# Performance work log

Hardware: AMD Instinct MI355X
Metric: run time of the kernel (lower is better)

## Reference

```python
import jax, jax.numpy as jnp
import numpy as np

EMBED_DIM = 1024
NUM_HEADS = 16
HEAD_DIM = EMBED_DIM // NUM_HEADS


def setup_inputs() -> dict:
    key = jax.random.key(0)
    k1, k2, k3, k4, k5 = jax.random.split(key, 5)
    B, T, C = 2, 2048, EMBED_DIM
    s = 1.0 / np.sqrt(C)
    return {
        "x": jax.random.normal(k1, (B, T, C), dtype=jnp.float32),
        "W_qkv": jax.random.normal(k2, (C, 3 * C), dtype=jnp.float32) * s,
        "b_qkv": jnp.zeros((3 * C,), dtype=jnp.float32),
        "W_out": jax.random.normal(k3, (C, C), dtype=jnp.float32) * s,
        "b_out": jnp.zeros((C,), dtype=jnp.float32),
    }


def reference(x, W_qkv, b_qkv, W_out, b_out):
    B, T, C = x.shape
    H, D = NUM_HEADS, HEAD_DIM
    qkv = x @ W_qkv + b_qkv                       # [B, T, 3C]
    q, k, v = jnp.split(qkv, 3, axis=-1)
    # [B, H, T, D]
    q = q.reshape(B, T, H, D).transpose(0, 2, 1, 3)
    k = k.reshape(B, T, H, D).transpose(0, 2, 1, 3)
    v = v.reshape(B, T, H, D).transpose(0, 2, 1, 3)
    scores = jnp.einsum("bhqd,bhkd->bhqk", q, k) / np.sqrt(D)  # [B,H,T,T]
    causal = jnp.tril(jnp.ones((T, T), dtype=bool))
    scores = jnp.where(causal[None, None], scores, -jnp.inf)
    weights = jax.nn.softmax(scores, axis=-1)
    out = jnp.einsum("bhqk,bhkd->bhqd", weights, v)  # [B,H,T,D]
    out = out.transpose(0, 2, 1, 3).reshape(B, T, C)
    return out @ W_out + b_out
```

## Files before the change

### kernel.cpp

```cpp
#include <hip/hip_runtime.h>
#include <stdint.h>

typedef unsigned short u16t;
typedef __attribute__((ext_vector_type(8))) short bf16x8;
typedef __attribute__((ext_vector_type(4))) float f32x4;

#define DEV __device__ __forceinline__

DEV u16t f2bf(float f) {
  union { float f; unsigned u; } v; v.f = f;
  unsigned r = v.u + 0x7FFFu + ((v.u >> 16) & 1u);
  return (u16t)(r >> 16);
}

DEV unsigned cvtpk(float a, float b) {
  unsigned r;
  asm("v_cvt_pk_bf16_f32 %0, %1, %2" : "=v"(r) : "v"(a), "v"(b));
  return r;
}

DEV void glds16(const void* g, void* l) {
  __builtin_amdgcn_global_load_lds((const __attribute__((address_space(1))) void*)g,
                                   (__attribute__((address_space(3))) void*)l, 16, 0, 0);
}

__global__ __launch_bounds__(256) void k_cast_x(const float* __restrict__ x,
                                                u16t* __restrict__ xb, int n) {
  int i = (blockIdx.x * 256 + threadIdx.x) * 8;
  if (i >= n) return;
  const float4* p = (const float4*)(x + i);
  float4 a = p[0], b = p[1];
  union { u16t h[8]; int4 v; } o;
  o.h[0] = f2bf(a.x); o.h[1] = f2bf(a.y); o.h[2] = f2bf(a.z); o.h[3] = f2bf(a.w);
  o.h[4] = f2bf(b.x); o.h[5] = f2bf(b.y); o.h[6] = f2bf(b.z); o.h[7] = f2bf(b.w);
  *(int4*)(xb + i) = o.v;
}

__global__ __launch_bounds__(256) void k_transpose_cast(const float* __restrict__ src,
                                                        u16t* __restrict__ dst,
                                                        int R, int C) {
  __shared__ u16t tile[64][65];
  int c0 = blockIdx.x * 64, r0 = blockIdx.y * 64;
  int tid = threadIdx.x;
#pragma unroll
  for (int i = 0; i < 16; i++) {
    int idx = tid + i * 256;
    int r = idx >> 6, c = idx & 63;
    tile[c][r] = f2bf(src[(size_t)(r0 + r) * C + (c0 + c)]);
  }
  __syncthreads();
#pragma unroll
  for (int i = 0; i < 16; i++) {
    int idx = tid + i * 256;
    int rr = idx >> 6, cc = idx & 63;
    dst[(size_t)(c0 + rr) * R + (r0 + cc)] = tile[rr][cc];
  }
}

template <int K>
DEV void gemm_mainloop(const u16t* __restrict__ A, const u16t* __restrict__ Bt,
                       int m0, int n0, u16t* ldsA, u16t* ldsB, f32x4 acc[4][4]) {
  const int tid = threadIdx.x;
  const int lane = tid & 63;
  const int wid = tid >> 6;
  const int wm = wid >> 1, wn = wid & 1;
#pragma unroll
  for (int i = 0; i < 4; i++)
#pragma unroll
    for (int j = 0; j < 4; j++) acc[i][j] = f32x4{0.f, 0.f, 0.f, 0.f};

  char* lA = (char*)ldsA;
  char* lB = (char*)ldsB;

  for (int k0 = 0; k0 < K; k0 += 32) {
#pragma unroll
    for (int j = 0; j < 2; j++) {
      int g = wid * 64 + lane + j * 256;
      int row = g >> 2;
      int cb = (g & 3) * 16;
      glds16((const char*)(A + (size_t)(m0 + row) * K + k0) + cb,
             lA + j * 4096 + wid * 1024);
      glds16((const char*)(Bt + (size_t)(n0 + row) * K + k0) + cb,
             lB + j * 4096 + wid * 1024);
    }
    __syncthreads();
    bf16x8 af[4], bfr[4];
    const int lr = lane & 15;
    const int ko = (lane >> 4) * 8;
#pragma unroll
    for (int f = 0; f < 4; f++) {
      af[f]  = *(const bf16x8*)(ldsA + (wm * 64 + f * 16 + lr) * 32 + ko);
      bfr[f] = *(const bf16x8*)(ldsB + (wn * 64 + f * 16 + lr) * 32 + ko);
    }
#pragma unroll
    for (int i = 0; i < 4; i++)
#pragma unroll
      for (int j = 0; j < 4; j++)
        acc[i][j] = __builtin_amdgcn_mfma_f32_16x16x32_bf16(af[i], bfr[j], acc[i][j], 0, 0, 0);
    __syncthreads();
  }
}

__global__ __launch_bounds__(256) void k_gemm_qkv(const u16t* __restrict__ xb,
                                                  const u16t* __restrict__ wt,
                                                  const float* __restrict__ bias,
                                                  u16t* __restrict__ q,
                                                  u16t* __restrict__ kk,
                                                  u16t* __restrict__ vt) {
  __shared__ u16t ldsA[128 * 32];
  __shared__ u16t ldsB[128 * 32];
  __shared__ u16t ldsE[4][64 * 64];
  const int m0 = blockIdx.x * 128, n0 = blockIdx.y * 128;
  f32x4 acc[4][4];
  gemm_mainloop<1024>(xb, wt, m0, n0, ldsA, ldsB, acc);

  const int lane = threadIdx.x & 63, wid = threadIdx.x >> 6;
  const int wm = wid >> 1, wn = wid & 1;
  const int nbase = n0 + wn * 64;
  const int which = nbase >> 10;
  const int hb = (nbase & 1023) >> 6;
  const int bb = m0 >> 11;
  const int t0 = (m0 & 2047) + wm * 64;
  const int bh = bb * 16 + hb;
  u16t* eb = ldsE[wid];
#pragma unroll
  for (int fm = 0; fm < 4; fm++) {
#pragma unroll
    for (int fn = 0; fn < 4; fn++) {
      float bv = bias[nbase + fn * 16 + (lane & 15)];
#pragma unroll
      for (int i = 0; i < 4; i++) {
        int t_loc = fm * 16 + (lane >> 4) * 4 + i;
        int d_loc = fn * 16 + (lane & 15);
        float v = acc[fm][fn][i] + bv;
        if (which == 2) eb[d_loc * 64 + t_loc] = f2bf(v);
        else            eb[t_loc * 64 + d_loc] = f2bf(v);
      }
    }
  }
  asm volatile("s_waitcnt lgkmcnt(0)" ::: "memory");
  u16t* dst;
  size_t base, rowstride;
  if (which == 2) { dst = vt; base = (size_t)bh * 64 * 2048 + t0; rowstride = 2048; }
  else { dst = (which == 0) ? q : kk; base = ((size_t)bh * 2048 + t0) * 64; rowstride = 64; }
#pragma unroll
  for (int it = 0; it < 8; it++) {
    int g = it * 64 + lane;
    int r = g >> 3;
    int ce = (g & 7) * 8;
    *(int4*)(dst + base + (size_t)r * rowstride + ce) = *(const int4*)(eb + r * 64 + ce);
  }
}

__global__ __launch_bounds__(128) void k_attn(const u16t* __restrict__ q,
                                              const u16t* __restrict__ kk,
                                              const u16t* __restrict__ vt,
                                              u16t* __restrict__ attn) {
  __shared__ u16t ldsK[128 * 64];
  __shared__ u16t ldsV[64 * 128];
  __shared__ u16t ldsP[2][16 * 128];
  const int p = blockIdx.x;
  const int t_lo = p, t_hi = 63 - p;
  const int lo_last = t_lo >> 2, hi_last = t_hi >> 2;
  const int bh = blockIdx.y;
  const int tid = threadIdx.x;
  const int lane = tid & 63, wid = tid >> 6;
  const int lr = lane & 15, lg = lane >> 4;
  const size_t hbase = (size_t)bh * 2048 * 64;
  const size_t vbase = (size_t)bh * 64 * 2048;
  const float NINF = -__builtin_inff();
  const float CEXP = 0.1803368801111204f;

  bf16x8 qlo[2], qhi[2];
  {
    const u16t* qp  = q + hbase + (size_t)(t_lo * 32 + wid * 16 + lr) * 64 + lg * 8;
    const u16t* qp2 = q + hbase + (size_t)(t_hi * 32 + wid * 16 + lr) * 64 + lg * 8;
#pragma unroll
    for (int ks = 0; ks < 2; ks++) {
      qlo[ks] = *(const bf16x8*)(qp + ks * 32);
      qhi[ks] = *(const bf16x8*)(qp2 + ks * 32);
    }
  }

  f32x4 olo[4], ohi[4];
#pragma unroll
  for (int i = 0; i < 4; i++) {
    olo[i] = f32x4{0.f, 0.f, 0.f, 0.f};
    ohi[i] = f32x4{0.f, 0.f, 0.f, 0.f};
  }
  float mlo = NINF, llo = 0.f, mhi = NINF, lhi = 0.f;

  u16t* pb = ldsP[wid];

  auto stage = [&](int kt) {
#pragma unroll
    for (int j = 0; j < 8; j++) {
      int g = j * 128 + tid;
      {
        int r = g >> 3;
        int cb = (g & 7) * 16;
        int sc = cb ^ ((r & 7) << 4);
        glds16((const char*)(kk + hbase + (size_t)(kt * 128 + r) * 64) + sc,
               (char*)ldsK + j * 2048 + wid * 1024);
      }
      {
        int r = g >> 4;
        int cb = (g & 15) * 16;
        int sc = cb ^ ((r & 7) << 4);
        glds16((const char*)(vt + vbase + (size_t)r * 2048 + kt * 128) + sc,
               (char*)ldsV + j * 2048 + wid * 1024);
      }
    }
  };

  auto compute = [&](bool diag, int moff, const bf16x8* qf, f32x4* o,
                     float& m_run, float& l_run) {
    const char* K = (const char*)ldsK;
    const char* V = (const char*)ldsV;
    float sv[8][4];
    __builtin_amdgcn_s_setprio(1);
#pragma unroll
    for (int f = 0; f < 8; f++) {
      f32x4 s = f32x4{0.f, 0.f, 0.f, 0.f};
#pragma unroll
      for (int ks = 0; ks < 2; ks++) {
        int row = f * 16 + lr;
        int cb = ks * 64 + lg * 16;
        bf16x8 kf = *(const bf16x8*)(K + row * 128 + (cb ^ ((row & 7) << 4)));
        s = __builtin_amdgcn_mfma_f32_16x16x32_bf16(kf, qf[ks], s, 0, 0, 0);
      }
#pragma unroll
      for (int i = 0; i < 4; i++) sv[f][i] = s[i];
    }
    __builtin_amdgcn_s_setprio(0);
    if (diag) {
      int qr = moff + wid * 16 + lr;
#pragma unroll
      for (int f = 0; f < 8; f++)
#pragma unroll
        for (int i = 0; i < 4; i++)
          if (f * 16 + lg * 4 + i > qr) sv[f][i] = NINF;
    }
    float fm[8];
#pragma unroll
    for (int f = 0; f < 8; f++)
      fm[f] = fmaxf(fmaxf(sv[f][0], sv[f][1]), fmaxf(sv[f][2], sv[f][3]));
    float mx = fmaxf(fmaxf(fmaxf(fm[0], fm[1]), fmaxf(fm[2], fm[3])),
                     fmaxf(fmaxf(fm[4], fm[5]), fmaxf(fm[6], fm[7])));
    mx = fmaxf(mx, __shfl_xor(mx, 16));
    mx = fmaxf(mx, __shfl_xor(mx, 32));
    if (!__all(mx <= m_run + 8.0f)) {
      float mnew = fmaxf(m_run, mx);
      float al = exp2f((m_run - mnew) * CEXP);
      m_run = mnew;
      l_run *= al;
#pragma unroll
      for (int df = 0; df < 4; df++)
#pragma unroll
        for (int i = 0; i < 4; i++) o[df][i] *= al;
    }
    const float nmc = -m_run * CEXP;
    float ps[8][4];
    float fs[8];
#pragma unroll
    for (int f = 0; f < 8; f++) {
#pragma unroll
      for (int i = 0; i < 4; i++)
        ps[f][i] = exp2f(__builtin_fmaf(sv[f][i], CEXP, nmc));
      fs[f] = (ps[f][0] + ps[f][1]) + (ps[f][2] + ps[f][3]);
    }
    float ssum = ((fs[0] + fs[1]) + (fs[2] + fs[3])) +
                 ((fs[4] + fs[5]) + (fs[6] + fs[7]));
    ssum += __shfl_xor(ssum, 16);
    ssum += __shfl_xor(ssum, 32);
    l_run += ssum;
#pragma unroll
    for (int f = 0; f < 8; f++) {
      union { unsigned u[2]; uint2 v; } pk;
      pk.u[0] = cvtpk(ps[f][0], ps[f][1]);
      pk.u[1] = cvtpk(ps[f][2], ps[f][3]);
      int cby = (f * 32 + lg * 8) ^ ((lr & 7) << 4);
      *(uint2*)((char*)pb + lr * 256 + cby) = pk.v;
    }
    asm volatile("s_waitcnt lgkmcnt(0)" ::: "memory");
    __builtin_amdgcn_s_setprio(1);
#pragma unroll
    for (int ks = 0; ks < 4; ks++) {
      int cb = ks * 64 + lg * 16;
      bf16x8 pf = *(const bf16x8*)((const char*)pb + lr * 256 + (cb ^ ((lr & 7) << 4)));
#pragma unroll
      for (int df = 0; df < 4; df++) {
        int vrow = df * 16 + lr;
        bf16x8 vf = *(const bf16x8*)(V + vrow * 256 + (cb ^ ((vrow & 7) << 4)));
        o[df] = __builtin_amdgcn_mfma_f32_16x16x32_bf16(vf, pf, o[df], 0, 0, 0);
      }
    }
    __builtin_amdgcn_s_setprio(0);
  };

  for (int kt = 0; kt <= hi_last; kt++) {
    stage(kt);
    __syncthreads();
    compute(kt == hi_last, (t_hi & 3) << 5, qhi, ohi, mhi, lhi);
    if (kt <= lo_last) compute(kt == lo_last, (t_lo & 3) << 5, qlo, olo, mlo, llo);
    __syncthreads();
  }

  const int bb = bh >> 4, h = bh & 15;
  auto epi = [&](int qt, const f32x4* o, float l_run) {
    float rinv = 1.0f / l_run;
    int t = qt * 32 + wid * 16 + lr;
    size_t rowb = ((size_t)bb * 2048 + t) * 1024 + h * 64;
#pragma unroll
    for (int df = 0; df < 4; df++) {
      union { unsigned u[2]; uint2 v; } pk;
      pk.u[0] = cvtpk(o[df][0] * rinv, o[df][1] * rinv);
      pk.u[1] = cvtpk(o[df][2] * rinv, o[df][3] * rinv);
      *(uint2*)(attn + rowb + df * 16 + lg * 4) = pk.v;
    }
  };
  epi(t_lo, olo, llo);
  epi(t_hi, ohi, lhi);
}

__global__ __launch_bounds__(256) void k_gemm_out(const u16t* __restrict__ attn,
                                                  const u16t* __restrict__ wt,
                                                  const float* __restrict__ bias,
                                                  float* __restrict__ out) {
  __shared__ u16t ldsA[128 * 32];
  __shared__ u16t ldsB[128 * 32];
  const int m0 = blockIdx.x * 128, n0 = blockIdx.y * 128;
  f32x4 acc[4][4];
  gemm_mainloop<1024>(attn, wt, m0, n0, ldsA, ldsB, acc);

  const int lane = threadIdx.x & 63, wid = threadIdx.x >> 6;
  const int wm = wid >> 1, wn = wid & 1;
#pragma unroll
  for (int fm = 0; fm < 4; fm++) {
    int row = m0 + wm * 64 + fm * 16 + (lane >> 4) * 4;
#pragma unroll
    for (int fn = 0; fn < 4; fn++) {
      int col = n0 + wn * 64 + fn * 16 + (lane & 15);
      float bv = bias[col];
#pragma unroll
      for (int i = 0; i < 4; i++)
        out[(size_t)(row + i) * 1024 + col] = acc[fm][fn][i] + bv;
    }
  }
}

extern "C" void kernel_launch(void* const* d_in, const int* in_sizes, int n_in,
                              void* d_out, int out_size, void* d_ws, size_t ws_size,
                              hipStream_t stream) {
  const float* x     = (const float*)d_in[0];
  const float* W_qkv = (const float*)d_in[1];
  const float* b_qkv = (const float*)d_in[2];
  const float* W_out = (const float*)d_in[3];
  const float* b_out = (const float*)d_in[4];
  float* out = (float*)d_out;

  char* ws = (char*)d_ws;
  u16t* xb    = (u16t*)(ws);
  u16t* wqkvT = (u16t*)(ws + 8388608);
  u16t* woutT = (u16t*)(ws + 14680064);
  u16t* qb    = (u16t*)(ws + 16777216);
  u16t* kb    = (u16t*)(ws + 25165824);
  u16t* vtb   = (u16t*)(ws + 33554432);
  u16t* attnb = (u16t*)(ws + 41943040);

  k_cast_x<<<2048, 256, 0, stream>>>(x, xb, 4194304);
  k_transpose_cast<<<dim3(48, 16), 256, 0, stream>>>(W_qkv, wqkvT, 1024, 3072);
  k_transpose_cast<<<dim3(16, 16), 256, 0, stream>>>(W_out, woutT, 1024, 1024);
  k_gemm_qkv<<<dim3(32, 24), 256, 0, stream>>>(xb, wqkvT, b_qkv, qb, kb, vtb);
  k_attn<<<dim3(32, 32), 128, 0, stream>>>(qb, kb, vtb, attnb);
  k_gemm_out<<<dim3(32, 8), 256, 0, stream>>>(attnb, woutT, b_out, out);
}
```

Baseline: 130.7 us.

## Template GEMM tile shape, shrink out-proj tile, swizzle blocks, alias LDS

The GEMM mainloop is templated on block tile size. The output projection now uses 128x64 tiles, giving 512 blocks instead of 256 so more CUs are busy. Both GEMMs use a 1D grid with a block-index swizzle so that co-scheduled blocks share operand tiles in cache. The QKV kernel reuses the mainloop LDS buffers for its epilogue staging, cutting shared memory to 32KB and possibly raising occupancy. Smaller tiles give less operand reuse per block.

```diff
diff --git a/kernel.cpp b/kernel.cpp
--- a/kernel.cpp
+++ b/kernel.cpp
@@ -57,45 +57,52 @@
   }
 }
 
-template <int K>
+template <int K, int BM, int BN>
 DEV void gemm_mainloop(const u16t* __restrict__ A, const u16t* __restrict__ Bt,
-                       int m0, int n0, u16t* ldsA, u16t* ldsB, f32x4 acc[4][4]) {
+                       int m0, int n0, u16t* ldsA, u16t* ldsB,
+                       f32x4 (&acc)[BM / 32][BN / 32]) {
+  constexpr int MF = BM / 32, NF = BN / 32;
   const int tid = threadIdx.x;
   const int lane = tid & 63;
   const int wid = tid >> 6;
   const int wm = wid >> 1, wn = wid & 1;
 #pragma unroll
-  for (int i = 0; i < 4; i++)
-#pragma unroll
-    for (int j = 0; j < 4; j++) acc[i][j] = f32x4{0.f, 0.f, 0.f, 0.f};
+  for (int i = 0; i < MF; i++)
+#pragma unroll
+    for (int j = 0; j < NF; j++) acc[i][j] = f32x4{0.f, 0.f, 0.f, 0.f};
 
   char* lA = (char*)ldsA;
   char* lB = (char*)ldsB;
 
   for (int k0 = 0; k0 < K; k0 += 32) {
 #pragma unroll
-    for (int j = 0; j < 2; j++) {
-      int g = wid * 64 + lane + j * 256;
+    for (int j = wid; j < BM / 16; j += 4) {
+      int g = j * 64 + lane;
       int row = g >> 2;
       int cb = (g & 3) * 16;
-      glds16((const char*)(A + (size_t)(m0 + row) * K + k0) + cb,
-             lA + j * 4096 + wid * 1024);
-      glds16((const char*)(Bt + (size_t)(n0 + row) * K + k0) + cb,
-             lB + j * 4096 + wid * 1024);
+      glds16((const char*)(A + (size_t)(m0 + row) * K + k0) + cb, lA + j * 1024);
+    }
+#pragma unroll
+    for (int j = wid; j < BN / 16; j += 4) {
+      int g = j * 64 + lane;
+      int row = g >> 2;
+      int cb = (g & 3) * 16;
+      glds16((const char*)(Bt + (size_t)(n0 + row) * K + k0) + cb, lB + j * 1024);
     }
     __syncthreads();
-    bf16x8 af[4], bfr[4];
+    bf16x8 af[MF], bfr[NF];
     const int lr = lane & 15;
     const int ko = (lane >> 4) * 8;
 #pragma unroll
-    for (int f = 0; f < 4; f++) {
-      af[f]  = *(const bf16x8*)(ldsA + (wm * 64 + f * 16 + lr) * 32 + ko);
-      bfr[f] = *(const bf16x8*)(ldsB + (wn * 64 + f * 16 + lr) * 32 + ko);
-    }
-#pragma unroll
-    for (int i = 0; i < 4; i++)
-#pragma unroll
-      for (int j = 0; j < 4; j++)
+    for (int f = 0; f < MF; f++)
+      af[f] = *(const bf16x8*)(ldsA + (wm * (BM / 2) + f * 16 + lr) * 32 + ko);
+#pragma unroll
+    for (int f = 0; f < NF; f++)
+      bfr[f] = *(const bf16x8*)(ldsB + (wn * (BN / 2) + f * 16 + lr) * 32 + ko);
+#pragma unroll
+    for (int i = 0; i < MF; i++)
+#pragma unroll
+      for (int j = 0; j < NF; j++)
         acc[i][j] = __builtin_amdgcn_mfma_f32_16x16x32_bf16(af[i], bfr[j], acc[i][j], 0, 0, 0);
     __syncthreads();
   }
@@ -107,12 +114,14 @@
                                                   u16t* __restrict__ q,
                                                   u16t* __restrict__ kk,
                                                   u16t* __restrict__ vt) {
-  __shared__ u16t ldsA[128 * 32];
-  __shared__ u16t ldsB[128 * 32];
-  __shared__ u16t ldsE[4][64 * 64];
-  const int m0 = blockIdx.x * 128, n0 = blockIdx.y * 128;
+  __shared__ char pool[32768];
+  u16t* ldsA = (u16t*)pool;
+  u16t* ldsB = (u16t*)(pool + 8192);
+  const int bid = blockIdx.x;
+  const int swz = (bid & 7) * 96 + (bid >> 3);
+  const int m0 = (swz & 31) * 128, n0 = (swz >> 5) * 128;
   f32x4 acc[4][4];
-  gemm_mainloop<1024>(xb, wt, m0, n0, ldsA, ldsB, acc);
+  gemm_mainloop<1024, 128, 128>(xb, wt, m0, n0, ldsA, ldsB, acc);
 
   const int lane = threadIdx.x & 63, wid = threadIdx.x >> 6;
   const int wm = wid >> 1, wn = wid & 1;
@@ -122,7 +131,7 @@
   const int bb = m0 >> 11;
   const int t0 = (m0 & 2047) + wm * 64;
   const int bh = bb * 16 + hb;
-  u16t* eb = ldsE[wid];
+  u16t* eb = (u16t*)(pool + wid * 8192);
 #pragma unroll
   for (int fm = 0; fm < 4; fm++) {
 #pragma unroll
@@ -328,10 +337,12 @@
                                                   const float* __restrict__ bias,
                                                   float* __restrict__ out) {
   __shared__ u16t ldsA[128 * 32];
-  __shared__ u16t ldsB[128 * 32];
-  const int m0 = blockIdx.x * 128, n0 = blockIdx.y * 128;
-  f32x4 acc[4][4];
-  gemm_mainloop<1024>(attn, wt, m0, n0, ldsA, ldsB, acc);
+  __shared__ u16t ldsB[64 * 32];
+  const int bid = blockIdx.x;
+  const int swz = (bid & 7) * 64 + (bid >> 3);
+  const int m0 = (swz & 31) * 128, n0 = (swz >> 5) * 64;
+  f32x4 acc[4][2];
+  gemm_mainloop<1024, 128, 64>(attn, wt, m0, n0, ldsA, ldsB, acc);
 
   const int lane = threadIdx.x & 63, wid = threadIdx.x >> 6;
   const int wm = wid >> 1, wn = wid & 1;
@@ -339,8 +350,8 @@
   for (int fm = 0; fm < 4; fm++) {
     int row = m0 + wm * 64 + fm * 16 + (lane >> 4) * 4;
 #pragma unroll
-    for (int fn = 0; fn < 4; fn++) {
-      int col = n0 + wn * 64 + fn * 16 + (lane & 15);
+    for (int fn = 0; fn < 2; fn++) {
+      int col = n0 + wn * 32 + fn * 16 + (lane & 15);
       float bv = bias[col];
 #pragma unroll
       for (int i = 0; i < 4; i++)
@@ -371,7 +382,7 @@
   k_cast_x<<<2048, 256, 0, stream>>>(x, xb, 4194304);
   k_transpose_cast<<<dim3(48, 16), 256, 0, stream>>>(W_qkv, wqkvT, 1024, 3072);
   k_transpose_cast<<<dim3(16, 16), 256, 0, stream>>>(W_out, woutT, 1024, 1024);
-  k_gemm_qkv<<<dim3(32, 24), 256, 0, stream>>>(xb, wqkvT, b_qkv, qb, kb, vtb);
+  k_gemm_qkv<<<768, 256, 0, stream>>>(xb, wqkvT, b_qkv, qb, kb, vtb);
   k_attn<<<dim3(32, 32), 128, 0, stream>>>(qb, kb, vtb, attnb);
-  k_gemm_out<<<dim3(32, 8), 256, 0, stream>>>(attnb, woutT, b_out, out);
-}
+  k_gemm_out<<<512, 256, 0, stream>>>(attnb, woutT, b_out, out);
+}
```

After: 135.7 us. 3.8% more time.
